# Optimization experiments

Measured on AMD Instinct MI355X. Metric: run time of the kernel, lower is better.

The kernel has to match this reference:

```python
import jax, jax.numpy as jnp
import numpy as np

B, NPER, K = 32, 256, 32
N, E = B * NPER, B * NPER * 32
H, NF, NG, L = 128, 128, 50, 6
CUTOFF = 10.0
LOG2 = 0.6931471805599453


def _ssp(x):
    # ShiftedSoftplus: softplus(x) - log(2)
    return jax.nn.softplus(x) - LOG2


def setup_inputs() -> dict:
    key = jax.random.key(0)
    ks = jax.random.split(key, 16)
    rng = np.random.default_rng(0)

    pos = jnp.asarray(rng.uniform(0.0, 5.0, size=(N, 3)).astype(np.float32))
    z = jnp.asarray(rng.integers(1, 100, size=(N,)).astype(np.int32))
    batch = jnp.asarray((np.arange(N) // NPER).astype(np.int32))
    # K neighbors per atom, within the same graph, no self-loops; dst sorted
    dst = np.repeat(np.arange(N), K)
    off = rng.integers(1, NPER, size=N * K)
    src = (dst % NPER + off) % NPER + (dst // NPER) * NPER
    edge_index = jnp.asarray(np.stack([src, dst]).astype(np.int32))
    domain_ids = jnp.asarray(rng.integers(0, 5, size=(B,)).astype(np.int32))

    def dense(k, i, o):
        return jax.random.normal(k, (i, o), jnp.float32) / np.sqrt(i)

    def stackw(k, i, o):
        return jax.random.normal(k, (L, i, o), jnp.float32) / np.sqrt(i)

    return {
        'pos': pos, 'z': z, 'batch': batch, 'edge_index': edge_index,
        'domain_ids': domain_ids,
        'embedding': jax.random.normal(ks[0], (100, H), jnp.float32),
        'mlp_w1': stackw(ks[1], NG, NF), 'mlp_b1': jnp.zeros((L, NF), jnp.float32),
        'mlp_w2': stackw(ks[2], NF, NF), 'mlp_b2': jnp.zeros((L, NF), jnp.float32),
        'cf_lin1_w': stackw(ks[3], H, NF),
        'cf_lin2_w': stackw(ks[4], NF, H), 'cf_lin2_b': jnp.zeros((L, H), jnp.float32),
        'int_lin_w': stackw(ks[5], H, H), 'int_lin_b': jnp.zeros((L, H), jnp.float32),
        'out_w1': dense(ks[6], H, H // 2), 'out_b1': jnp.zeros((H // 2,), jnp.float32),
        'out_w2': dense(ks[7], H // 2, 1), 'out_b2': jnp.zeros((1,), jnp.float32),
        'dom_emb': jax.random.normal(ks[8], (5, 64), jnp.float32),
        'film_w1': dense(ks[9], 64, 128), 'film_b1': jnp.zeros((128,), jnp.float32),
        'film_w2': dense(ks[10], 128, 128), 'film_b2': jnp.zeros((128,), jnp.float32),
        'gamma_w': dense(ks[11], 128, H), 'gamma_b': jnp.zeros((H,), jnp.float32),
        'beta_w': dense(ks[12], 128, H), 'beta_b': jnp.zeros((H,), jnp.float32),
    }


def reference(pos, z, batch, edge_index, domain_ids, embedding,
              mlp_w1, mlp_b1, mlp_w2, mlp_b2, cf_lin1_w, cf_lin2_w, cf_lin2_b,
              int_lin_w, int_lin_b, out_w1, out_b1, out_w2, out_b2,
              dom_emb, film_w1, film_b1, film_w2, film_b2,
              gamma_w, gamma_b, beta_w, beta_b):
    n_atoms = pos.shape[0]
    n_graphs = domain_ids.shape[0]
    src, dst = edge_index[0], edge_index[1]

    # edge distances, gaussian smearing, cosine cutoff (computed once)
    d = jnp.sqrt(jnp.sum((pos[src] - pos[dst]) ** 2, axis=-1))          # [E]
    offsets = jnp.linspace(0.0, CUTOFF, NG).astype(pos.dtype)
    coeff = -0.5 / (CUTOFF / (NG - 1)) ** 2
    edge_attr = jnp.exp(coeff * (d[:, None] - offsets) ** 2)            # [E,NG]
    C = 0.5 * (jnp.cos(d * (np.pi / CUTOFF)) + 1.0)                     # [E]

    h = embedding[z]                                                    # [N,H]
    for l in range(L):
        # filter network on gaussian basis, modulated by cosine cutoff
        W = (_ssp(edge_attr @ mlp_w1[l] + mlp_b1[l]) @ mlp_w2[l] + mlp_b2[l]) * C[:, None]  # [E,NF]
        x = h @ cf_lin1_w[l]                                            # [N,NF]
        msg = x[src] * W                                                # [E,NF]
        agg = jax.ops.segment_sum(msg, dst, num_segments=n_atoms)       # [N,NF]
        x = agg @ cf_lin2_w[l] + cf_lin2_b[l]                           # [N,H]
        h = h + _ssp(x) @ int_lin_w[l] + int_lin_b[l]                   # residual

    atom_e = _ssp(h @ out_w1 + out_b1) @ out_w2 + out_b2                # [N,1]
    e_graph = jax.ops.segment_sum(atom_e, batch, num_segments=n_graphs) # [B,1]

    # FiLM domain bias (features are zeros, so gamma path contributes 0 - faithful)
    de = dom_emb[domain_ids]                                            # [B,64]
    film = jax.nn.relu(de @ film_w1 + film_b1) @ film_w2 + film_b2      # [B,128]
    gamma = film @ gamma_w + gamma_b                                    # [B,H]
    beta = film @ beta_w + beta_b                                       # [B,H]
    dummy = jnp.zeros((n_graphs, H), pos.dtype)
    bias = jnp.sum(gamma * dummy + beta, axis=-1)                       # [B]

    # faithful broadcast [B,1]+[B] -> [B,B], then sum(dim=1) as in original
    energy = jnp.sum(e_graph + bias[None, :], axis=1)                   # [B]

    forces = jnp.zeros((n_atoms, 3), energy.dtype)
    stress = jnp.zeros((n_graphs, 3, 3), energy.dtype)
    features = jnp.zeros((n_atoms, H), energy.dtype)
    return energy, forces, stress, features
```

## Files before the change

### kernel.cpp

```cpp
#include <hip/hip_runtime.h>
#include <math.h>

using uint = unsigned int;
typedef _Float16 h2    __attribute__((ext_vector_type(2)));
typedef _Float16 f16x8 __attribute__((ext_vector_type(8)));
typedef float    f32x4 __attribute__((ext_vector_type(4)));

#define N_ATOMS 8192
#define NEDGE   262144
#define KNBR    32
#define NGAUSS  50
#define NLAYER  6
#define NB      32
#define GTAB    1024
#define DMAX    8.6603f
#define FCUT    10.0f
#define MB      1048576

#define LSTRIDE 76
#define S_WT    0
#define S_AS    9728

#define WA_OFF  0
#define WB_OFF  8192
#define AS_OFF  16384
#define TS_OFF  17408
#define LAY_N   18432

#define T_W1    0
#define T_W2    4096
#define T_RBF   12288
#define T_HID   13312
#define TAB_SMEM 15360

#define OW1P_OFF 147456
#define M1_OFF   151552
#define M2_OFF   176128
#define WPACK_N  225280

__device__ __forceinline__ float ssp(float x) {
    return fmaxf(x, 0.0f) + log1pf(expf(-fabsf(x))) - 0.69314718055994531f;
}
__device__ __forceinline__ uint pack2(float a, float b) {
    union { h2 h; uint u; } x;
    h2 v; v.x = (_Float16)a; v.y = (_Float16)b; x.h = v; return x.u;
}
__device__ __forceinline__ h2 u2h(uint u) {
    union { uint u; h2 h; } x; x.u = u; return x.h;
}
__device__ __forceinline__ uint h2u(h2 h) {
    union { h2 h; uint u; } x; x.h = h; return x.u;
}
__device__ __forceinline__ float fdot2f(h2 a, h2 b, float c) {
#if __has_builtin(__builtin_amdgcn_fdot2)
    return __builtin_amdgcn_fdot2(a, b, c, false);
#else
    return fmaf((float)a.y, (float)b.y, fmaf((float)a.x, (float)b.x, c));
#endif
}

__device__ __forceinline__ int swz(int row, int quad) {
    return row * 64 + ((quad ^ (row & 15)) << 2);
}
__device__ __forceinline__ int swzc(int row, int c) {
    return row * 64 + (((c >> 2) ^ (row & 15)) << 2) + (c & 3);
}

__device__ __forceinline__ void stage_sw(uint* dst, const uint* __restrict__ src,
                                         int n16, int tid) {
    for (int i = tid; i < n16; i += 256) {
        uint4 v = ((const uint4*)src)[i];
        *(uint4*)&dst[swz(i >> 4, i & 15)] = v;
    }
}

template<int NCT>
__device__ __forceinline__ void run_gemm_sw(const uint* smA, const uint* smW,
                                            int lane, int nb, f32x4* acc) {
    int m = lane & 15, q = lane >> 4;
    #pragma unroll
    for (int ks = 0; ks < 4; ++ks) {
        int cq = q + ks * 4;
        f16x8 a = *(const f16x8*)&smA[swz(m, cq)];
        #pragma unroll
        for (int ct = 0; ct < NCT; ++ct) {
            int n = nb + ct * 16 + m;
            f16x8 b = *(const f16x8*)&smW[swz(n, cq)];
            acc[ct] = __builtin_amdgcn_mfma_f32_16x16x32_f16(a, b, acc[ct], 0, 0, 0);
        }
    }
}

template<int NCT>
__device__ __forceinline__ void run_gemm(const uint* sm, int as_off, int lane,
                                         int nb, f32x4* acc) {
    int m = lane & 15, q = lane >> 4;
    #pragma unroll
    for (int ks = 0; ks < 4; ++ks) {
        f16x8 a = *(const f16x8*)&sm[as_off + m * LSTRIDE + q * 4 + ks * 16];
        #pragma unroll
        for (int ct = 0; ct < NCT; ++ct) {
            f16x8 b = *(const f16x8*)&sm[S_WT + (nb + ct * 16 + m) * LSTRIDE + q * 4 + ks * 16];
            acc[ct] = __builtin_amdgcn_mfma_f32_16x16x32_f16(a, b, acc[ct], 0, 0, 0);
        }
    }
}

struct SArgs {
    const float *pos; const int *z; const int *ei; const int *dom;
    const float *emb;
    const float *cf1; const float *cf2w; const float *intw; const float *ow1;
    const float *mw1; const float *mw2;
    const float *dome; const float *fw1; const float *fb1;
    const float *fw2; const float *fb2; const float *bw; const float *bb;
    uint2 *epack; float *h; uint *xA;
    float *gbias; uint *wpack; float *out; int out_size;
};

__global__ void __launch_bounds__(256) k_setup(SArgs a) {
    __shared__ __align__(16) uint sm[S_AS + 1216];
    const int tid = threadIdx.x, bid = blockIdx.x;
    const int gidx = bid * 256 + tid, gsz = 512 * 256;
    const int lane = tid & 63, w = tid >> 6;
    const int m = lane & 15, q = lane >> 4;
    const int rowbase = bid * 16;

    for (int i = gidx; i < a.out_size; i += gsz) a.out[i] = 0.0f;

    for (int idx = gidx; idx < WPACK_N; idx += gsz) {
        if (idx < OW1P_OFF) {
            int mat = idx >> 13, e = idx & 8191;
            int kp = e >> 7, cc = e & 127;
            const float* src = (mat < 6) ? (a.cf1 + mat * 16384)
                            : (mat < 12) ? (a.cf2w + (mat - 6) * 16384)
                                         : (a.intw + (mat - 12) * 16384);
            a.wpack[mat * 8192 + cc * 64 + kp] =
                pack2(src[2 * kp * 128 + cc], src[(2 * kp + 1) * 128 + cc]);
        } else if (idx < M1_OFF) {
            int e = idx - OW1P_OFF;
            int kp = e >> 6, cc = e & 63;
            a.wpack[OW1P_OFF + cc * 64 + kp] =
                pack2(a.ow1[2 * kp * 64 + cc], a.ow1[(2 * kp + 1) * 64 + cc]);
        } else if (idx < M2_OFF) {
            int e = idx - M1_OFF;
            int l = e >> 12, r = e & 4095;
            int kp = r >> 7, cc = r & 127;
            int g0 = 2 * kp;
            float va = (g0 < NGAUSS)     ? a.mw1[l*NGAUSS*128 + g0*128 + cc]     : 0.f;
            float vb = (g0 + 1 < NGAUSS) ? a.mw1[l*NGAUSS*128 + (g0+1)*128 + cc] : 0.f;
            a.wpack[idx] = pack2(va, vb);
        } else {
            int e = idx - M2_OFF;
            int l = e >> 13, r = e & 8191;
            int kp = r >> 7, cc = r & 127;
            a.wpack[idx] = pack2(a.mw2[l*16384 + 2*kp*128 + cc],
                                 a.mw2[l*16384 + (2*kp+1)*128 + cc]);
        }
    }

    const float invdelta = (float)(GTAB - 1) / DMAX;
    #pragma unroll
    for (int t = 0; t < 2; ++t) {
        int e = rowbase * KNBR + t * 256 + tid;
        int s = a.ei[e], d = a.ei[NEDGE + e];
        float dx = a.pos[3*s] - a.pos[3*d];
        float dy = a.pos[3*s+1] - a.pos[3*d+1];
        float dz = a.pos[3*s+2] - a.pos[3*d+2];
        float dist = sqrtf(dx*dx + dy*dy + dz*dz);
        float u = dist * invdelta;
        int i0 = (int)u; i0 = (i0 < GTAB - 2) ? i0 : (GTAB - 2);
        float t2 = u - (float)i0;
        uint tb = pack2(t2, 0.0f) & 0xffffu;
        uint2 ep; ep.x = (uint)s; ep.y = (tb << 16) | (uint)i0;
        a.epack[e] = ep;
    }

    for (int i = tid; i < 1024; i += 256) {
        int r = i >> 6, f2 = i & 63;
        int zz = a.z[rowbase + r];
        float2 v = *(const float2*)&a.emb[zz * 128 + f2 * 2];
        *(float2*)&a.h[(rowbase + r) * 128 + f2 * 2] = v;
        sm[S_AS + r * LSTRIDE + f2] = pack2(v.x, v.y);
    }
    for (int i = tid; i < 2048; i += 256) {
        int m4 = i >> 7, cc = i & 127;
        float v[8];
        #pragma unroll
        for (int j = 0; j < 8; ++j) v[j] = a.cf1[(8 * m4 + j) * 128 + cc];
        uint4 pk; pk.x = pack2(v[0], v[1]); pk.y = pack2(v[2], v[3]);
        pk.z = pack2(v[4], v[5]); pk.w = pack2(v[6], v[7]);
        *(uint4*)&sm[cc * LSTRIDE + m4 * 4] = pk;
    }
    __syncthreads();
    {
        f32x4 acc[2] = {{0,0,0,0},{0,0,0,0}};
        run_gemm<2>(sm, S_AS, lane, w * 32, acc);
        #pragma unroll
        for (int ct = 0; ct < 2; ++ct) {
            int n = w * 32 + ct * 16 + m;
            #pragma unroll
            for (int i = 0; i < 4; ++i) {
                float v = acc[ct][i];
                float u = __shfl_xor(v, 1, 64);
                if (!(lane & 1))
                    a.xA[(rowbase + q * 4 + i) * 64 + (n >> 1)] = pack2(v, u);
            }
        }
    }
    __syncthreads();
    if (bid >= 32 && bid < 64) {
        int g = bid - 32;
        float* fs = (float*)sm;
        if (tid < 64) fs[tid] = a.dome[a.dom[g] * 64 + tid];
        __syncthreads();
        if (tid < 128) {
            float acc = a.fb1[tid];
            for (int i = 0; i < 64; ++i) acc = fmaf(fs[i], a.fw1[i*128 + tid], acc);
            fs[64 + tid] = fmaxf(acc, 0.0f);
        }
        __syncthreads();
        if (tid < 128) {
            float acc = a.fb2[tid];
            for (int i = 0; i < 128; ++i) acc = fmaf(fs[64+i], a.fw2[i*128 + tid], acc);
            fs[192 + tid] = acc;
        }
        __syncthreads();
        if (tid < 128) {
            float acc = a.bb[tid];
            for (int i = 0; i < 128; ++i) acc = fmaf(fs[192+i], a.bw[i*128 + tid], acc);
            #pragma unroll
            for (int off = 32; off > 0; off >>= 1) acc += __shfl_down(acc, off, 64);
            if ((tid & 63) == 0) fs[320 + (tid >> 6)] = acc;
        }
        __syncthreads();
        if (tid == 0) a.gbias[g] = fs[320] + fs[321];
    }
}

__global__ void __launch_bounds__(256) k_table(
    const uint* __restrict__ wpack, const float* __restrict__ mb1,
    const float* __restrict__ mb2, uint* __restrict__ tab2) {
    __shared__ __align__(16) uint sm[TAB_SMEM];
    const int tid = threadIdx.x;
    const int l = blockIdx.x >> 5;
    const int base = (blockIdx.x & 31) * 32;
    { const uint4* s4 = (const uint4*)(wpack + M1_OFF + l*4096);
      uint4* d4 = (uint4*)&sm[T_W1];
      for (int i = tid; i < 1024; i += 256) d4[i] = s4[i]; }
    { const uint4* s4 = (const uint4*)(wpack + M2_OFF + l*8192);
      uint4* d4 = (uint4*)&sm[T_W2];
      for (int i = tid; i < 2048; i += 256) d4[i] = s4[i]; }
    const float delta = DMAX / (float)(GTAB - 1);
    const float gstep = FCUT / (float)(NGAUSS - 1);
    const float coeff = -0.5f / (gstep * gstep);
    for (int i = tid; i < 1024; i += 256) {
        int r = i >> 5, kp = i & 31;
        float dv = (float)(base + r) * delta;
        int g0 = 2 * kp;
        float v0 = 0.f, v1 = 0.f;
        if (g0 < NGAUSS)     { float t = dv - (float)g0 * gstep;     v0 = expf(coeff*t*t); }
        if (g0 + 1 < NGAUSS) { float t = dv - (float)(g0+1) * gstep; v1 = expf(coeff*t*t); }
        sm[T_RBF + i] = pack2(v0, v1);
    }
    __syncthreads();
    int tx = tid & 31, ty = tid >> 5, c0 = tx * 4, tr0 = ty * 4;
    float acc[4][4];
    #pragma unroll
    for (int i = 0; i < 4; ++i) { acc[i][0]=0.f; acc[i][1]=0.f; acc[i][2]=0.f; acc[i][3]=0.f; }
    #pragma unroll
    for (int oct = 0; oct < 8; ++oct) {
        int kp0 = oct * 4;
        uint4 w_[4];
        #pragma unroll
        for (int p = 0; p < 4; ++p) w_[p] = *(const uint4*)&sm[T_W1 + (kp0+p)*128 + c0];
        #pragma unroll
        for (int i = 0; i < 4; ++i) {
            uint4 av = *(const uint4*)&sm[T_RBF + (tr0+i)*32 + kp0];
            uint aa[4] = {av.x, av.y, av.z, av.w};
            #pragma unroll
            for (int p = 0; p < 4; ++p) {
                h2 ap = u2h(aa[p]);
                acc[i][0] = fdot2f(ap, u2h(w_[p].x), acc[i][0]);
                acc[i][1] = fdot2f(ap, u2h(w_[p].y), acc[i][1]);
                acc[i][2] = fdot2f(ap, u2h(w_[p].z), acc[i][2]);
                acc[i][3] = fdot2f(ap, u2h(w_[p].w), acc[i][3]);
            }
        }
    }
    float4 b1v = *(const float4*)&mb1[l*128 + c0];
    #pragma unroll
    for (int i = 0; i < 4; ++i) {
        uint2 o;
        o.x = pack2(ssp(acc[i][0] + b1v.x), ssp(acc[i][1] + b1v.y));
        o.y = pack2(ssp(acc[i][2] + b1v.z), ssp(acc[i][3] + b1v.w));
        *(uint2*)&sm[T_HID + (tr0+i)*64 + (c0 >> 1)] = o;
    }
    __syncthreads();
    float acc2[4][4];
    #pragma unroll
    for (int i = 0; i < 4; ++i) { acc2[i][0]=0.f; acc2[i][1]=0.f; acc2[i][2]=0.f; acc2[i][3]=0.f; }
    #pragma unroll 4
    for (int oct = 0; oct < 16; ++oct) {
        int kp0 = oct * 4;
        uint4 w_[4];
        #pragma unroll
        for (int p = 0; p < 4; ++p) w_[p] = *(const uint4*)&sm[T_W2 + (kp0+p)*128 + c0];
        #pragma unroll
        for (int i = 0; i < 4; ++i) {
            uint4 av = *(const uint4*)&sm[T_HID + (tr0+i)*64 + kp0];
            uint aa[4] = {av.x, av.y, av.z, av.w};
            #pragma unroll
            for (int p = 0; p < 4; ++p) {
                h2 ap = u2h(aa[p]);
                acc2[i][0] = fdot2f(ap, u2h(w_[p].x), acc2[i][0]);
                acc2[i][1] = fdot2f(ap, u2h(w_[p].y), acc2[i][1]);
                acc2[i][2] = fdot2f(ap, u2h(w_[p].z), acc2[i][2]);
                acc2[i][3] = fdot2f(ap, u2h(w_[p].w), acc2[i][3]);
            }
        }
    }
    float4 b2v = *(const float4*)&mb2[l*128 + c0];
    #pragma unroll
    for (int i = 0; i < 4; ++i) {
        int row = base + tr0 + i;
        float dv = (float)row * delta;
        float Cd = 0.5f * (cosf(dv * 0.3141592653589793f) + 1.0f);
        uint2 o;
        o.x = pack2((acc2[i][0] + b2v.x)*Cd, (acc2[i][1] + b2v.y)*Cd);
        o.y = pack2((acc2[i][2] + b2v.z)*Cd, (acc2[i][3] + b2v.w)*Cd);
        *(uint2*)&tab2[(l*GTAB + row)*128 + tx*4] = o;
        if (row > 0)
            *(uint2*)&tab2[(l*GTAB + row - 1)*128 + tx*4 + 2] = o;
    }
}

template<bool LAST>
__global__ void __launch_bounds__(256) k_layer(
    float* __restrict__ h, const uint* __restrict__ xin, uint* __restrict__ xout,
    const uint* __restrict__ tab2l, const uint2* __restrict__ epack,
    const uint* __restrict__ w2p, const uint* __restrict__ w3p,
    const uint* __restrict__ w1np,
    const float* __restrict__ b2, const float* __restrict__ b3,
    const float* __restrict__ ob1, const float* __restrict__ ow2,
    const float* __restrict__ ob2, const float* __restrict__ gbias,
    float* __restrict__ out) {
    __shared__ __align__(16) uint sm[LAY_N];
    const int tid = threadIdx.x, bid = blockIdx.x;
    const int lane = tid & 63, w = tid >> 6;
    const int m = lane & 15, q = lane >> 4;
    const int rowbase = bid * 16;

    float hr[2][4];
    #pragma unroll
    for (int ct = 0; ct < 2; ++ct)
        #pragma unroll
        for (int i = 0; i < 4; ++i)
            hr[ct][i] = h[(rowbase + q * 4 + i) * 128 + w * 32 + ct * 16 + m];

    stage_sw(&sm[WA_OFF], w2p, 2048, tid);
    {
        const int side = lane >> 5, l5 = lane & 31;
        #pragma unroll
        for (int p = 0; p < 4; ++p) {
            int al = p * 4 + w;
            uint2 ep = epack[(rowbase + al) * KNBR + l5];
            h2 a0; a0.x = (_Float16)0; a0.y = (_Float16)0;
            h2 a1 = a0;
            #pragma unroll 4
            for (int k = 0; k < 16; ++k) {
                int e = 2 * k + side;
                uint s = __shfl(ep.x, e, 64);
                uint y = __shfl(ep.y, e, 64);
                int i0 = (int)(y & 0xffffu);
                uint th = y >> 16;
                h2 t2 = u2h(th | (th << 16));
                uint4 tv = *(const uint4*)&tab2l[i0 * 128 + l5 * 4];
                uint2 xv = *(const uint2*)&xin[s * 64 + l5 * 2];
                h2 w0 = u2h(tv.x) + t2 * (u2h(tv.z) - u2h(tv.x));
                h2 w1 = u2h(tv.y) + t2 * (u2h(tv.w) - u2h(tv.y));
                a0 = a0 + u2h(xv.x) * w0;
                a1 = a1 + u2h(xv.y) * w1;
            }
            uint u0 = h2u(a0), u1 = h2u(a1);
            uint p0 = __shfl_xor(u0, 32, 64), p1 = __shfl_xor(u1, 32, 64);
            if (side == 0) {
                h2 r0 = u2h(u0) + u2h(p0), r1 = u2h(u1) + u2h(p1);
                uint2 o; o.x = h2u(r0); o.y = h2u(r1);
                *(uint2*)&sm[AS_OFF + swzc(al, l5 * 2)] = o;
            }
        }
    }
    __syncthreads();
    stage_sw(&sm[WB_OFF], w3p, 2048, tid);
    {
        f32x4 acc[2] = {{0,0,0,0},{0,0,0,0}};
        run_gemm_sw<2>(&sm[AS_OFF], &sm[WA_OFF], lane, w * 32, acc);
        #pragma unroll
        for (int ct = 0; ct < 2; ++ct) {
            int n = w * 32 + ct * 16 + m;
            float bv = b2[n];
            #pragma unroll
            for (int i = 0; i < 4; ++i) {
                float v = ssp(acc[ct][i] + bv);
                float u = __shfl_xor(v, 1, 64);
                if (!(lane & 1))
                    sm[TS_OFF + swzc(q * 4 + i, n >> 1)] = pack2(v, u);
            }
        }
    }
    __syncthreads();
    stage_sw(&sm[WA_OFF], w1np, LAST ? 1024 : 2048, tid);
    {
        f32x4 acc[2] = {{0,0,0,0},{0,0,0,0}};
        run_gemm_sw<2>(&sm[TS_OFF], &sm[WB_OFF], lane, w * 32, acc);
        #pragma unroll
        for (int ct = 0; ct < 2; ++ct) {
            int n = w * 32 + ct * 16 + m;
            float bv = b3[n];
            #pragma unroll
            for (int i = 0; i < 4; ++i) {
                int r = rowbase + q * 4 + i;
                float hv = hr[ct][i] + acc[ct][i] + bv;
                h[r * 128 + n] = hv;
                float u = __shfl_xor(hv, 1, 64);
                if (!(lane & 1))
                    sm[AS_OFF + swzc(q * 4 + i, n >> 1)] = pack2(hv, u);
            }
        }
    }
    __syncthreads();
    if (!LAST) {
        f32x4 acc[2] = {{0,0,0,0},{0,0,0,0}};
        run_gemm_sw<2>(&sm[AS_OFF], &sm[WA_OFF], lane, w * 32, acc);
        #pragma unroll
        for (int ct = 0; ct < 2; ++ct) {
            int n = w * 32 + ct * 16 + m;
            #pragma unroll
            for (int i = 0; i < 4; ++i) {
                float v = acc[ct][i];
                float u = __shfl_xor(v, 1, 64);
                if (!(lane & 1))
                    xout[(rowbase + q * 4 + i) * 64 + (n >> 1)] = pack2(v, u);
            }
        }
    } else {
        f32x4 acc[1] = {{0,0,0,0}};
        run_gemm_sw<1>(&sm[AS_OFF], &sm[WA_OFF], lane, w * 16, acc);
        int n = w * 16 + m;
        float b1v = ob1[n], w2v = ow2[n];
        float part = 0.f;
        #pragma unroll
        for (int i = 0; i < 4; ++i) part += ssp(acc[0][i] + b1v) * w2v;
        #pragma unroll
        for (int mm = 1; mm < 64; mm <<= 1) part += __shfl_xor(part, mm, 64);
        float* fs = (float*)&sm[TS_OFF];
        if (lane == 0) fs[w] = part;
        __syncthreads();
        if (tid == 0) {
            float bsum = fs[0] + fs[1] + fs[2] + fs[3] + 16.0f * ob2[0];
            float add = 32.0f * bsum;
            if ((bid & 15) == 0) {
                float sb = 0.f;
                for (int j = 0; j < NB; ++j) sb += gbias[j];
                add += sb;
            }
            atomicAdd(&out[bid >> 4], add);
        }
    }
}

extern "C" void kernel_launch(void* const* d_in, const int* in_sizes, int n_in,
                              void* d_out, int out_size, void* d_ws, size_t ws_size,
                              hipStream_t stream) {
    SArgs a;
    a.pos  = (const float*)d_in[0];
    a.z    = (const int*)d_in[1];
    a.ei   = (const int*)d_in[3];
    a.dom  = (const int*)d_in[4];
    a.emb  = (const float*)d_in[5];
    a.mw1  = (const float*)d_in[6];
    const float* mb1 = (const float*)d_in[7];
    a.mw2  = (const float*)d_in[8];
    const float* mb2 = (const float*)d_in[9];
    a.cf1  = (const float*)d_in[10];
    a.cf2w = (const float*)d_in[11];
    const float* cf2b = (const float*)d_in[12];
    a.intw = (const float*)d_in[13];
    const float* intb = (const float*)d_in[14];
    a.ow1  = (const float*)d_in[15];
    const float* ob1  = (const float*)d_in[16];
    const float* ow2  = (const float*)d_in[17];
    const float* ob2  = (const float*)d_in[18];
    a.dome = (const float*)d_in[19];
    a.fw1  = (const float*)d_in[20];
    a.fb1  = (const float*)d_in[21];
    a.fw2  = (const float*)d_in[22];
    a.fb2  = (const float*)d_in[23];
    a.bw   = (const float*)d_in[26];
    a.bb   = (const float*)d_in[27];

    char* ws = (char*)d_ws;
    a.epack   = (uint2*)(ws + 0);
    uint* tab2= (uint*)(ws + 2*MB);
    a.h       = (float*)(ws + 5*MB);
    a.xA      = (uint*)(ws + 9*MB);
    uint* xB  = (uint*)(ws + 11*MB);
    a.gbias   = (float*)(ws + 15*MB);
    a.wpack   = (uint*)(ws + 15*MB + 4096);
    a.out = (float*)d_out;
    a.out_size = out_size;

    k_setup<<<512, 256, 0, stream>>>(a);
    k_table<<<192, 256, 0, stream>>>(a.wpack, mb1, mb2, tab2);

    const uint* xr = a.xA;
    uint* xw = xB;
    for (int l = 0; l < NLAYER; ++l) {
        const uint* w2p = a.wpack + (6 + l) * 8192;
        const uint* w3p = a.wpack + (12 + l) * 8192;
        if (l < NLAYER - 1) {
            k_layer<false><<<512, 256, 0, stream>>>(
                a.h, xr, xw, tab2 + l*GTAB*128, a.epack, w2p, w3p,
                a.wpack + (l + 1) * 8192,
                cf2b + l*128, intb + l*128, ob1, ow2, ob2, a.gbias, a.out);
        } else {
            k_layer<true><<<512, 256, 0, stream>>>(
                a.h, xr, xw, tab2 + l*GTAB*128, a.epack, w2p, w3p,
                a.wpack + OW1P_OFF,
                cf2b + l*128, intb + l*128, ob1, ow2, ob2, a.gbias, a.out);
        }
        const uint* tmp = xr; xr = xw; xw = (uint*)tmp;
    }
}
```

Before: 267.0 us.

## Fuse all interaction layers into one persistent per-graph kernel

```diff
diff --git a/kernel.cpp b/kernel.cpp
--- a/kernel.cpp
+++ b/kernel.cpp
@@ -21,11 +21,8 @@
 #define S_WT    0
 #define S_AS    9728
 
-#define WA_OFF  0
-#define WB_OFF  8192
-#define AS_OFF  16384
-#define TS_OFF  17408
-#define LAY_N   18432
+#define GW_OFF  0
+#define GAS_OFF 8192
 
 #define T_W1    0
 #define T_W2    4096
@@ -69,6 +66,13 @@
 __device__ __forceinline__ void stage_sw(uint* dst, const uint* __restrict__ src,
                                          int n16, int tid) {
     for (int i = tid; i < n16; i += 256) {
+        uint4 v = ((const uint4*)src)[i];
+        *(uint4*)&dst[swz(i >> 4, i & 15)] = v;
+    }
+}
+__device__ __forceinline__ void stage_g(uint* dst, const uint* __restrict__ src,
+                                        int n16, int tid) {
+    for (int i = tid; i < n16; i += 1024) {
         uint4 v = ((const uint4*)src)[i];
         *(uint4*)&dst[swz(i >> 4, i & 15)] = v;
     }
@@ -334,36 +338,31 @@
     }
 }
 
-template<bool LAST>
-__global__ void __launch_bounds__(256) k_layer(
-    float* __restrict__ h, const uint* __restrict__ xin, uint* __restrict__ xout,
-    const uint* __restrict__ tab2l, const uint2* __restrict__ epack,
-    const uint* __restrict__ w2p, const uint* __restrict__ w3p,
-    const uint* __restrict__ w1np,
-    const float* __restrict__ b2, const float* __restrict__ b3,
+__global__ void __launch_bounds__(1024) k_graph(
+    float* __restrict__ h, uint* __restrict__ x,
+    const uint* __restrict__ tab2, const uint2* __restrict__ epack,
+    const uint* __restrict__ wpack,
+    const float* __restrict__ cf2b, const float* __restrict__ intb,
     const float* __restrict__ ob1, const float* __restrict__ ow2,
     const float* __restrict__ ob2, const float* __restrict__ gbias,
     float* __restrict__ out) {
-    __shared__ __align__(16) uint sm[LAY_N];
-    const int tid = threadIdx.x, bid = blockIdx.x;
-    const int lane = tid & 63, w = tid >> 6;
+    __shared__ __align__(16) uint sm[24576];
+    const int tid = threadIdx.x;
+    const int g = blockIdx.x;
+    const int wave = tid >> 6, lane = tid & 63;
     const int m = lane & 15, q = lane >> 4;
-    const int rowbase = bid * 16;
-
-    float hr[2][4];
-    #pragma unroll
-    for (int ct = 0; ct < 2; ++ct)
-        #pragma unroll
-        for (int i = 0; i < 4; ++i)
-            hr[ct][i] = h[(rowbase + q * 4 + i) * 128 + w * 32 + ct * 16 + m];
-
-    stage_sw(&sm[WA_OFF], w2p, 2048, tid);
-    {
-        const int side = lane >> 5, l5 = lane & 31;
-        #pragma unroll
-        for (int p = 0; p < 4; ++p) {
-            int al = p * 4 + w;
-            uint2 ep = epack[(rowbase + al) * KNBR + l5];
+    const int side = lane >> 5, l5 = lane & 31;
+    uint* As = &sm[GAS_OFF + wave * 1024];
+    const int arow0 = g * 256 + wave * 16;
+
+    for (int l = 0; l < NLAYER; ++l) {
+        const uint* tab2l = tab2 + l * GTAB * 128;
+        const float* b2 = cf2b + l * 128;
+        const float* b3 = intb + l * 128;
+        stage_g(&sm[GW_OFF], wpack + (6 + l) * 8192, 2048, tid);
+        for (int p = 0; p < 16; ++p) {
+            int atom = arow0 + p;
+            uint2 ep = epack[atom * KNBR + l5];
             h2 a0; a0.x = (_Float16)0; a0.y = (_Float16)0;
             h2 a1 = a0;
             #pragma unroll 4
@@ -375,7 +374,7 @@
                 uint th = y >> 16;
                 h2 t2 = u2h(th | (th << 16));
                 uint4 tv = *(const uint4*)&tab2l[i0 * 128 + l5 * 4];
-                uint2 xv = *(const uint2*)&xin[s * 64 + l5 * 2];
+                uint2 xv = *(const uint2*)&x[s * 64 + l5 * 2];
                 h2 w0 = u2h(tv.x) + t2 * (u2h(tv.z) - u2h(tv.x));
                 h2 w1 = u2h(tv.y) + t2 * (u2h(tv.w) - u2h(tv.y));
                 a0 = a0 + u2h(xv.x) * w0;
@@ -386,85 +385,102 @@
             if (side == 0) {
                 h2 r0 = u2h(u0) + u2h(p0), r1 = u2h(u1) + u2h(p1);
                 uint2 o; o.x = h2u(r0); o.y = h2u(r1);
-                *(uint2*)&sm[AS_OFF + swzc(al, l5 * 2)] = o;
-            }
-        }
-    }
-    __syncthreads();
-    stage_sw(&sm[WB_OFF], w3p, 2048, tid);
-    {
-        f32x4 acc[2] = {{0,0,0,0},{0,0,0,0}};
-        run_gemm_sw<2>(&sm[AS_OFF], &sm[WA_OFF], lane, w * 32, acc);
-        #pragma unroll
-        for (int ct = 0; ct < 2; ++ct) {
-            int n = w * 32 + ct * 16 + m;
-            float bv = b2[n];
-            #pragma unroll
-            for (int i = 0; i < 4; ++i) {
-                float v = ssp(acc[ct][i] + bv);
-                float u = __shfl_xor(v, 1, 64);
-                if (!(lane & 1))
-                    sm[TS_OFF + swzc(q * 4 + i, n >> 1)] = pack2(v, u);
-            }
-        }
-    }
-    __syncthreads();
-    stage_sw(&sm[WA_OFF], w1np, LAST ? 1024 : 2048, tid);
-    {
-        f32x4 acc[2] = {{0,0,0,0},{0,0,0,0}};
-        run_gemm_sw<2>(&sm[TS_OFF], &sm[WB_OFF], lane, w * 32, acc);
-        #pragma unroll
-        for (int ct = 0; ct < 2; ++ct) {
-            int n = w * 32 + ct * 16 + m;
-            float bv = b3[n];
-            #pragma unroll
-            for (int i = 0; i < 4; ++i) {
-                int r = rowbase + q * 4 + i;
-                float hv = hr[ct][i] + acc[ct][i] + bv;
-                h[r * 128 + n] = hv;
-                float u = __shfl_xor(hv, 1, 64);
-                if (!(lane & 1))
-                    sm[AS_OFF + swzc(q * 4 + i, n >> 1)] = pack2(hv, u);
-            }
-        }
-    }
-    __syncthreads();
-    if (!LAST) {
-        f32x4 acc[2] = {{0,0,0,0},{0,0,0,0}};
-        run_gemm_sw<2>(&sm[AS_OFF], &sm[WA_OFF], lane, w * 32, acc);
-        #pragma unroll
-        for (int ct = 0; ct < 2; ++ct) {
-            int n = w * 32 + ct * 16 + m;
-            #pragma unroll
-            for (int i = 0; i < 4; ++i) {
-                float v = acc[ct][i];
-                float u = __shfl_xor(v, 1, 64);
-                if (!(lane & 1))
-                    xout[(rowbase + q * 4 + i) * 64 + (n >> 1)] = pack2(v, u);
-            }
-        }
-    } else {
-        f32x4 acc[1] = {{0,0,0,0}};
-        run_gemm_sw<1>(&sm[AS_OFF], &sm[WA_OFF], lane, w * 16, acc);
-        int n = w * 16 + m;
-        float b1v = ob1[n], w2v = ow2[n];
-        float part = 0.f;
-        #pragma unroll
-        for (int i = 0; i < 4; ++i) part += ssp(acc[0][i] + b1v) * w2v;
-        #pragma unroll
-        for (int mm = 1; mm < 64; mm <<= 1) part += __shfl_xor(part, mm, 64);
-        float* fs = (float*)&sm[TS_OFF];
-        if (lane == 0) fs[w] = part;
-        __syncthreads();
-        if (tid == 0) {
-            float bsum = fs[0] + fs[1] + fs[2] + fs[3] + 16.0f * ob2[0];
-            float add = 32.0f * bsum;
-            if ((bid & 15) == 0) {
+                *(uint2*)&As[swzc(p, l5 * 2)] = o;
+            }
+        }
+        __syncthreads();
+        {
+            f32x4 acc[8];
+            #pragma unroll
+            for (int i = 0; i < 8; ++i) acc[i] = (f32x4){0,0,0,0};
+            run_gemm_sw<8>(As, &sm[GW_OFF], lane, 0, acc);
+            #pragma unroll
+            for (int ct = 0; ct < 8; ++ct) {
+                int n = ct * 16 + m;
+                float bv = b2[n];
+                #pragma unroll
+                for (int i = 0; i < 4; ++i) {
+                    float v = ssp(acc[ct][i] + bv);
+                    float u = __shfl_xor(v, 1, 64);
+                    if (!(m & 1))
+                        As[swzc(q * 4 + i, n >> 1)] = pack2(v, u);
+                }
+            }
+        }
+        __syncthreads();
+        stage_g(&sm[GW_OFF], wpack + (12 + l) * 8192, 2048, tid);
+        __syncthreads();
+        {
+            f32x4 acc[8];
+            #pragma unroll
+            for (int i = 0; i < 8; ++i) acc[i] = (f32x4){0,0,0,0};
+            run_gemm_sw<8>(As, &sm[GW_OFF], lane, 0, acc);
+            #pragma unroll
+            for (int ct = 0; ct < 8; ++ct) {
+                int n = ct * 16 + m;
+                float bv = b3[n];
+                #pragma unroll
+                for (int i = 0; i < 4; ++i) {
+                    int r = arow0 + q * 4 + i;
+                    float hv = h[r * 128 + n] + acc[ct][i] + bv;
+                    h[r * 128 + n] = hv;
+                    float u = __shfl_xor(hv, 1, 64);
+                    if (!(m & 1))
+                        As[swzc(q * 4 + i, n >> 1)] = pack2(hv, u);
+                }
+            }
+        }
+        __syncthreads();
+        if (l < NLAYER - 1) {
+            stage_g(&sm[GW_OFF], wpack + (l + 1) * 8192, 2048, tid);
+            __syncthreads();
+            f32x4 acc[8];
+            #pragma unroll
+            for (int i = 0; i < 8; ++i) acc[i] = (f32x4){0,0,0,0};
+            run_gemm_sw<8>(As, &sm[GW_OFF], lane, 0, acc);
+            #pragma unroll
+            for (int ct = 0; ct < 8; ++ct) {
+                int n = ct * 16 + m;
+                #pragma unroll
+                for (int i = 0; i < 4; ++i) {
+                    float v = acc[ct][i];
+                    float u = __shfl_xor(v, 1, 64);
+                    if (!(m & 1))
+                        x[(arow0 + q * 4 + i) * 64 + (n >> 1)] = pack2(v, u);
+                }
+            }
+            __syncthreads();
+        } else {
+            stage_g(&sm[GW_OFF], wpack + OW1P_OFF, 1024, tid);
+            __syncthreads();
+            f32x4 acc[4];
+            #pragma unroll
+            for (int i = 0; i < 4; ++i) acc[i] = (f32x4){0,0,0,0};
+            run_gemm_sw<4>(As, &sm[GW_OFF], lane, 0, acc);
+            float part = 0.f;
+            #pragma unroll
+            for (int ct = 0; ct < 4; ++ct) {
+                int n = ct * 16 + m;
+                float b1v = ob1[n], w2v = ow2[n];
+                #pragma unroll
+                for (int i = 0; i < 4; ++i)
+                    part += ssp(acc[ct][i] + b1v) * w2v;
+            }
+            #pragma unroll
+            for (int mm = 1; mm < 64; mm <<= 1) part += __shfl_xor(part, mm, 64);
+            __syncthreads();
+            float* fs = (float*)&sm[GW_OFF];
+            if (lane == 0) fs[wave] = part;
+            __syncthreads();
+            if (tid == 0) {
+                float tot = 0.f;
+                #pragma unroll
+                for (int i = 0; i < 16; ++i) tot += fs[i];
+                tot += 256.0f * ob2[0];
                 float sb = 0.f;
                 for (int j = 0; j < NB; ++j) sb += gbias[j];
-                add += sb;
-            }
-            atomicAdd(&out[bid >> 4], add);
+                out[g] = 32.0f * tot + sb;
+            }
         }
     }
 }
@@ -504,7 +520,6 @@
     uint* tab2= (uint*)(ws + 2*MB);
     a.h       = (float*)(ws + 5*MB);
     a.xA      = (uint*)(ws + 9*MB);
-    uint* xB  = (uint*)(ws + 11*MB);
     a.gbias   = (float*)(ws + 15*MB);
     a.wpack   = (uint*)(ws + 15*MB + 4096);
     a.out = (float*)d_out;
@@ -512,23 +527,7 @@
 
     k_setup<<<512, 256, 0, stream>>>(a);
     k_table<<<192, 256, 0, stream>>>(a.wpack, mb1, mb2, tab2);
-
-    const uint* xr = a.xA;
-    uint* xw = xB;
-    for (int l = 0; l < NLAYER; ++l) {
-        const uint* w2p = a.wpack + (6 + l) * 8192;
-        const uint* w3p = a.wpack + (12 + l) * 8192;
-        if (l < NLAYER - 1) {
-            k_layer<false><<<512, 256, 0, stream>>>(
-                a.h, xr, xw, tab2 + l*GTAB*128, a.epack, w2p, w3p,
-                a.wpack + (l + 1) * 8192,
-                cf2b + l*128, intb + l*128, ob1, ow2, ob2, a.gbias, a.out);
-        } else {
-            k_layer<true><<<512, 256, 0, stream>>>(
-                a.h, xr, xw, tab2 + l*GTAB*128, a.epack, w2p, w3p,
-                a.wpack + OW1P_OFF,
-                cf2b + l*128, intb + l*128, ob1, ow2, ob2, a.gbias, a.out);
-        }
-        const uint* tmp = xr; xr = xw; xw = (uint*)tmp;
-    }
-}
+    k_graph<<<NB, 1024, 0, stream>>>(a.h, a.xA, tab2, a.epack, a.wpack,
+                                     cf2b, intb, ob1, ow2, ob2, a.gbias,
+                                     (float*)d_out);
+}
```

Result: slower. 891.4 us (+233.9%).
